# Kernel tuning notes

Hardware: AMD Instinct MI355X
Metric: run time of the kernel (lower is better)

The kernel has to match this reference:

```python
import jax, jax.numpy as jnp
import numpy as np

WS = 7          # window size
DIM = 256       # channels
HEADS = 8       # attention heads
NW = 1024       # windows per image ((224/7)^2)
B = 4           # image batch
N = WS * WS     # tokens per window


def get_relative_position_index(ws):
    # Faithful numpy port of the torch helper for square equal q/k windows.
    coords = np.stack(np.meshgrid(np.arange(ws), np.arange(ws), indexing='ij'))  # (2, ws, ws)
    flat = coords.reshape(2, -1)                                                  # (2, N)
    rel = flat[:, :, None] - flat[:, None, :]                                     # (2, N, N)
    rel = rel.transpose(1, 2, 0).astype(np.int32)                                 # (N, N, 2)
    rel[..., 0] += ws - 1
    rel[..., 1] += ws - 1
    rel[..., 0] *= 2 * ws - 1   # q_windows[1] + k_windows[1] - 1
    return rel.sum(-1)          # (N, N) in [0, (2*ws-1)^2)


def setup_inputs() -> dict:
    key = jax.random.key(0)
    ks = jax.random.split(key, 8)
    B_ = B * NW
    x = jax.random.normal(ks[0], (B_, N, DIM), dtype=jnp.float32)
    mask = jax.random.normal(ks[1], (NW, N, N), dtype=jnp.float32)  # additive window mask
    qkv_w = jax.random.normal(ks[2], (3 * DIM, DIM), dtype=jnp.float32) * (DIM ** -0.5)
    qkv_b = jax.random.normal(ks[3], (3 * DIM,), dtype=jnp.float32) * 0.02
    proj_w = jax.random.normal(ks[4], (DIM, DIM), dtype=jnp.float32) * (DIM ** -0.5)
    proj_b = jax.random.normal(ks[5], (DIM,), dtype=jnp.float32) * 0.02
    rpb_table = jax.random.normal(ks[6], ((2 * WS - 1) ** 2, HEADS), dtype=jnp.float32) * 0.02
    rel_pos_index = jnp.asarray(get_relative_position_index(WS), dtype=jnp.int32)
    return {"x": x, "mask": mask, "qkv_w": qkv_w, "qkv_b": qkv_b,
            "proj_w": proj_w, "proj_b": proj_b,
            "rpb_table": rpb_table, "rel_pos_index": rel_pos_index}


def reference(x, mask, qkv_w, qkv_b, proj_w, proj_b, rpb_table, rel_pos_index):
    B_, n, C = x.shape
    hd = C // HEADS
    scale = hd ** -0.5
    # qkv projection: (B_, N, 3, H, hd) -> (3, B_, H, N, hd)
    qkv = (x @ qkv_w.T + qkv_b).reshape(B_, n, 3, HEADS, hd).transpose(2, 0, 3, 1, 4)
    q, k, v = qkv[0] * scale, qkv[1], qkv[2]
    attn = jnp.einsum('bhnd,bhmd->bhnm', q, k)                  # (B_, H, N, N)
    bias = rpb_table[rel_pos_index].transpose(2, 0, 1)          # gather -> (H, N, N)
    attn = attn + bias[None]
    nW = mask.shape[0]
    attn = attn.reshape(B_ // nW, nW, HEADS, n, n) + mask[None, :, None]
    attn = jax.nn.softmax(attn.reshape(B_, HEADS, n, n), axis=-1)
    out = jnp.einsum('bhnm,bhmd->bhnd', attn, v)                # (B_, H, N, hd)
    out = out.transpose(0, 2, 1, 3).reshape(B_, n, C)
    return out @ proj_w.T + proj_b
```

## Files before the change

kernel.cpp:

```cpp
#include <hip/hip_runtime.h>

typedef short bf16x8 __attribute__((ext_vector_type(8)));
typedef unsigned short u16x8 __attribute__((ext_vector_type(8)));
typedef unsigned short u16x4 __attribute__((ext_vector_type(4)));
typedef float f32x4 __attribute__((ext_vector_type(4)));
typedef unsigned short u16;

#define N_TOK 49
#define DIM   256
#define NWIN  1024
#define XS_S  264
#define QK_S  40
#define VT_S  72
#define P_S   72
#define OH_S  40

#define WS_MASK_OFF   0ull
#define WS_QKVW_OFF   2458624ull
#define WS_PROJW_OFF  (WS_QKVW_OFF + 196608ull)
#define WS_QKVB_OFF   (WS_PROJW_OFF + 65536ull)
#define WS_PROJB_OFF  (WS_QKVB_OFF + 768ull)
#define WS_RPB_OFF    (WS_PROJB_OFF + 256ull)
#define WS_TOT_U16    (WS_RPB_OFF + 1352ull)

__device__ __forceinline__ float bf2f(u16 b) {
  unsigned int u = ((unsigned int)b) << 16;
  return __builtin_bit_cast(float, u);
}
__device__ __forceinline__ u16 f2bf(float f) {
  unsigned int u = __builtin_bit_cast(unsigned int, f);
  return (u16)((u + 0x7fffu + ((u >> 16) & 1u)) >> 16);
}
__device__ __forceinline__ float lde(const void* p, size_t i, bool isbf) {
  return isbf ? bf2f(((const u16*)p)[i]) : ((const float*)p)[i];
}
__device__ __forceinline__ bf16x8 cvt8(const float* f) {
  f32x4 a = *(const f32x4*)f;
  f32x4 b = *(const f32x4*)(f + 4);
  u16x8 r;
  r[0]=f2bf(a[0]); r[1]=f2bf(a[1]); r[2]=f2bf(a[2]); r[3]=f2bf(a[3]);
  r[4]=f2bf(b[0]); r[5]=f2bf(b[1]); r[6]=f2bf(b[2]); r[7]=f2bf(b[3]);
  return __builtin_bit_cast(bf16x8, r);
}
__device__ __forceinline__ bool probe_bf(const void* p) {
  int lane = threadIdx.x & 63;
  u16 h = ((const u16*)p)[2 * lane];
  int e = (h >> 7) & 0xFF;
  bool sane = ((h & 0x7fffu) == 0) || (e >= 96 && e <= 140);
  return (__ballot(!sane) == 0ull);
}

__global__ void cvt_kernel(const void* __restrict__ src, u16* __restrict__ dst, int n) {
  bool isbf = probe_bf(src);
  int i = blockIdx.x * 256 + threadIdx.x;
  if (i < n)
    dst[i] = isbf ? ((const u16*)src)[i] : f2bf(((const float*)src)[i]);
}

__global__ __launch_bounds__(256, 2)
void winattn_kernel(const void* __restrict__ x, const void* __restrict__ mask,
                    const void* __restrict__ qkv_w, const void* __restrict__ qkv_b,
                    const void* __restrict__ proj_w, const void* __restrict__ proj_b,
                    const void* __restrict__ rpb, const int* __restrict__ rel_idx,
                    void* __restrict__ out, const u16* __restrict__ wsu, int use_ws)
{
  __shared__ u16 xs [64 * XS_S];
  __shared__ u16 qs [64 * QK_S];
  __shared__ u16 ksm[64 * QK_S];
  __shared__ u16 vT [32 * VT_S];
  __shared__ u16 Ps [64 * P_S];
  __shared__ u16 oh [64 * OH_S];

  const int tid  = threadIdx.x;
  const int wv   = tid >> 6;
  const int lane = tid & 63;
  const int quad = lane >> 4;
  const int l15  = lane & 15;
  const int w    = blockIdx.x;

  const bool bx = probe_bf(x);
  bool bm0 = probe_bf(mask), bw0 = probe_bf(qkv_w), bqb0 = probe_bf(qkv_b),
       bpw0 = probe_bf(proj_w), bpb0 = probe_bf(proj_b), brp0 = probe_bf(rpb);

  const void* mask_p = use_ws ? (const void*)(wsu + WS_MASK_OFF)  : mask;
  const void* qkvw_p = use_ws ? (const void*)(wsu + WS_QKVW_OFF)  : qkv_w;
  const void* qkvb_p = use_ws ? (const void*)(wsu + WS_QKVB_OFF)  : qkv_b;
  const void* pjw_p  = use_ws ? (const void*)(wsu + WS_PROJW_OFF) : proj_w;
  const void* pjb_p  = use_ws ? (const void*)(wsu + WS_PROJB_OFF) : proj_b;
  const void* rpb_p  = use_ws ? (const void*)(wsu + WS_RPB_OFF)   : rpb;
  const bool bm  = use_ws ? true : bm0;
  const bool bw  = use_ws ? true : bw0;
  const bool bqb = use_ws ? true : bqb0;
  const bool bpw = use_ws ? true : bpw0;
  const bool bpb = use_ws ? true : bpb0;
  const bool brp = use_ws ? true : brp0;

  if (bx) {
    const u16* xw = (const u16*)x + (size_t)w * (N_TOK * DIM);
    for (int c = tid; c < (N_TOK * DIM / 8); c += 256) {
      int t = (c * 8) >> 8, col = (c * 8) & 255;
      *(u16x8*)&xs[t * XS_S + col] = ((const u16x8*)xw)[c];
    }
  } else {
    const float* xw = (const float*)x + (size_t)w * (N_TOK * DIM);
    for (int c = tid; c < (N_TOK * DIM / 8); c += 256) {
      int t = (c * 8) >> 8, col = (c * 8) & 255;
      *(u16x8*)&xs[t * XS_S + col] = __builtin_bit_cast(u16x8, cvt8(xw + c * 8));
    }
  }
  {
    u16x8 z = {0, 0, 0, 0, 0, 0, 0, 0};
    for (int c = tid; c < 495; c += 256)
      *(u16x8*)&xs[N_TOK * XS_S + c * 8] = z;
  }
  __syncthreads();

  f32x4 pacc[16];
  #pragma unroll
  for (int i = 0; i < 16; ++i) pacc[i] = (f32x4){0.f, 0.f, 0.f, 0.f};

  const int    mrow = 16 * wv + quad * 4;
  const size_t moff = (size_t)(w & (NWIN - 1)) * (N_TOK * N_TOK);

  #pragma unroll 1
  for (int h = 0; h < 8; ++h) {
    f32x4 acc[6];
    #pragma unroll
    for (int j = 0; j < 6; ++j) acc[j] = (f32x4){0.f, 0.f, 0.f, 0.f};
    const int  nb0  = h * 32;
    const u16* arow = &xs[(16 * wv + l15) * XS_S + quad * 8];
    if (bw) {
      const u16* wp = (const u16*)qkvw_p;
      #pragma unroll
      for (int ks = 0; ks < 8; ++ks) {
        bf16x8 a = *(const bf16x8*)(arow + ks * 32);
        #pragma unroll
        for (int j = 0; j < 6; ++j) {
          int n = (j >> 1) * 256 + nb0 + (j & 1) * 16 + l15;
          bf16x8 b = *(const bf16x8*)(wp + (size_t)n * DIM + ks * 32 + quad * 8);
          acc[j] = __builtin_amdgcn_mfma_f32_16x16x32_bf16(a, b, acc[j], 0, 0, 0);
        }
      }
    } else {
      const float* wp = (const float*)qkvw_p;
      #pragma unroll
      for (int ks = 0; ks < 8; ++ks) {
        bf16x8 a = *(const bf16x8*)(arow + ks * 32);
        #pragma unroll
        for (int j = 0; j < 6; ++j) {
          int n = (j >> 1) * 256 + nb0 + (j & 1) * 16 + l15;
          bf16x8 b = cvt8(wp + (size_t)n * DIM + ks * 32 + quad * 8);
          acc[j] = __builtin_amdgcn_mfma_f32_16x16x32_bf16(a, b, acc[j], 0, 0, 0);
        }
      }
    }
    {
      const float scale = 0.1767766952966369f;
      #pragma unroll
      for (int j = 0; j < 6; ++j) {
        int   n    = (j >> 1) * 256 + nb0 + (j & 1) * 16 + l15;
        float bias = lde(qkvb_p, n, bqb);
        int   lc   = (j & 1) * 16 + l15;
        if (j < 2) {
          #pragma unroll
          for (int r = 0; r < 4; ++r)
            qs[(mrow + r) * QK_S + lc] = f2bf((acc[j][r] + bias) * scale);
        } else if (j < 4) {
          #pragma unroll
          for (int r = 0; r < 4; ++r)
            ksm[(mrow + r) * QK_S + lc] = f2bf(acc[j][r] + bias);
        } else {
          u16x4 pk;
          #pragma unroll
          for (int r = 0; r < 4; ++r) pk[r] = f2bf(acc[j][r] + bias);
          *(u16x4*)&vT[lc * VT_S + mrow] = pk;
        }
      }
    }
    __syncthreads();

    f32x4 s[4];
    {
      bf16x8 aq = *(const bf16x8*)&qs[(16 * wv + l15) * QK_S + quad * 8];
      #pragma unroll
      for (int ni = 0; ni < 4; ++ni) {
        bf16x8 bk = *(const bf16x8*)&ksm[(ni * 16 + l15) * QK_S + quad * 8];
        s[ni] = __builtin_amdgcn_mfma_f32_16x16x32_bf16(aq, bk, (f32x4){0.f,0.f,0.f,0.f}, 0, 0, 0);
      }
    }
    float rs[4];
    #pragma unroll
    for (int r = 0; r < 4; ++r) {
      int m = mrow + r;
      #pragma unroll
      for (int ni = 0; ni < 4; ++ni) {
        int   n = ni * 16 + l15;
        float v = s[ni][r];
        if (n >= N_TOK) {
          v = -1e30f;
        } else if (m < N_TOK) {
          int idx = rel_idx[m * N_TOK + n];
          v += lde(rpb_p, (size_t)idx * 8 + h, brp) + lde(mask_p, moff + m * N_TOK + n, bm);
        }
        s[ni][r] = v;
      }
      float mx = fmaxf(fmaxf(s[0][r], s[1][r]), fmaxf(s[2][r], s[3][r]));
      #pragma unroll
      for (int d2 = 1; d2 < 16; d2 <<= 1) mx = fmaxf(mx, __shfl_xor(mx, d2));
      float sum = 0.f;
      #pragma unroll
      for (int ni = 0; ni < 4; ++ni) {
        float p = __expf(s[ni][r] - mx);
        s[ni][r] = p;
        sum += p;
      }
      #pragma unroll
      for (int d2 = 1; d2 < 16; d2 <<= 1) sum += __shfl_xor(sum, d2);
      rs[r] = sum;
      #pragma unroll
      for (int ni = 0; ni < 4; ++ni)
        Ps[(mrow + r) * P_S + ni * 16 + l15] = f2bf(s[ni][r]);
    }

    f32x4 o0 = {0.f,0.f,0.f,0.f}, o1 = {0.f,0.f,0.f,0.f};
    #pragma unroll
    for (int ks = 0; ks < 2; ++ks) {
      bf16x8 ap = *(const bf16x8*)&Ps[(16 * wv + l15) * P_S + ks * 32 + quad * 8];
      bf16x8 b0 = *(const bf16x8*)&vT[(l15)      * VT_S + ks * 32 + quad * 8];
      bf16x8 b1 = *(const bf16x8*)&vT[(16 + l15) * VT_S + ks * 32 + quad * 8];
      o0 = __builtin_amdgcn_mfma_f32_16x16x32_bf16(ap, b0, o0, 0, 0, 0);
      o1 = __builtin_amdgcn_mfma_f32_16x16x32_bf16(ap, b1, o1, 0, 0, 0);
    }
    #pragma unroll
    for (int r = 0; r < 4; ++r) {
      float inv = 1.f / rs[r];
      oh[(mrow + r) * OH_S + l15]      = f2bf(o0[r] * inv);
      oh[(mrow + r) * OH_S + 16 + l15] = f2bf(o1[r] * inv);
    }

    {
      bf16x8 ao = *(const bf16x8*)&oh[(16 * wv + l15) * OH_S + quad * 8];
      if (bpw) {
        const u16* pp = (const u16*)pjw_p;
        #pragma unroll
        for (int ni = 0; ni < 16; ++ni) {
          bf16x8 bp = *(const bf16x8*)(pp + (size_t)(ni * 16 + l15) * DIM + h * 32 + quad * 8);
          pacc[ni] = __builtin_amdgcn_mfma_f32_16x16x32_bf16(ao, bp, pacc[ni], 0, 0, 0);
        }
      } else {
        const float* pp = (const float*)pjw_p;
        #pragma unroll
        for (int ni = 0; ni < 16; ++ni) {
          bf16x8 bp = cvt8(pp + (size_t)(ni * 16 + l15) * DIM + h * 32 + quad * 8);
          pacc[ni] = __builtin_amdgcn_mfma_f32_16x16x32_bf16(ao, bp, pacc[ni], 0, 0, 0);
        }
      }
    }
    __syncthreads();
  }

  const size_t obase = (size_t)w * (N_TOK * DIM);
  if (bx) {
    u16* ow = (u16*)out + obase;
    #pragma unroll
    for (int r = 0; r < 4; ++r) {
      int m = mrow + r;
      if (m < N_TOK) {
        #pragma unroll
        for (int ni = 0; ni < 16; ++ni) {
          int col = ni * 16 + l15;
          ow[m * DIM + col] = f2bf(pacc[ni][r] + lde(pjb_p, col, bpb));
        }
      }
    }
  } else {
    float* ow = (float*)out + obase;
    #pragma unroll
    for (int r = 0; r < 4; ++r) {
      int m = mrow + r;
      if (m < N_TOK) {
        #pragma unroll
        for (int ni = 0; ni < 16; ++ni) {
          int col = ni * 16 + l15;
          ow[m * DIM + col] = pacc[ni][r] + lde(pjb_p, col, bpb);
        }
      }
    }
  }
}

extern "C" void kernel_launch(void* const* d_in, const int* in_sizes, int n_in,
                              void* d_out, int out_size, void* d_ws, size_t ws_size,
                              hipStream_t stream) {
  const int use_ws = (ws_size >= WS_TOT_U16 * 2) ? 1 : 0;
  u16* wsu = (u16*)d_ws;
  if (use_ws) {
    auto cv = [&](const void* src, unsigned long long off, int n) {
      cvt_kernel<<<(n + 255) / 256, 256, 0, stream>>>(src, wsu + off, n);
    };
    cv(d_in[1], WS_MASK_OFF,  NWIN * N_TOK * N_TOK);
    cv(d_in[2], WS_QKVW_OFF,  3 * DIM * DIM);
    cv(d_in[3], WS_QKVB_OFF,  3 * DIM);
    cv(d_in[4], WS_PROJW_OFF, DIM * DIM);
    cv(d_in[5], WS_PROJB_OFF, DIM);
    cv(d_in[6], WS_RPB_OFF,   169 * 8);
  }
  winattn_kernel<<<4096, 256, 0, stream>>>(
      d_in[0], d_in[1], d_in[2], d_in[3], d_in[4], d_in[5], d_in[6],
      (const int*)d_in[7], d_out, wsu, use_ws);
}
```

Before: 1.824 ms.

## Precombine mask and position bias per head, keep x in registers, double-buffer QKV

A new preprocessing kernel fuses the window mask and the gathered relative-position bias into one bf16 table per window and head. The attention kernel then loads that table with a single read per element instead of an index gather plus two lookups. The x tile now lives in registers rather than LDS. The q/k/v LDS buffers are double-buffered so the per-head trailing barrier can be removed, and launch bounds rise to 3 blocks per SM. In exchange the bias table is about 39 MB of extra workspace traffic, and register pressure goes up.

```diff
diff --git a/kernel.cpp b/kernel.cpp
--- a/kernel.cpp
+++ b/kernel.cpp
@@ -7,9 +7,9 @@
 typedef unsigned short u16;
 
 #define N_TOK 49
+#define NN    2401
 #define DIM   256
 #define NWIN  1024
-#define XS_S  264
 #define QK_S  40
 #define VT_S  72
 #define P_S   72
@@ -23,6 +23,13 @@
 #define WS_RPB_OFF    (WS_PROJB_OFF + 256ull)
 #define WS_TOT_U16    (WS_RPB_OFF + 1352ull)
 
+#define C2_CMB_OFF    0ull
+#define C2_QKVW_OFF   (1024ull * 8ull * NN)
+#define C2_PROJW_OFF  (C2_QKVW_OFF + 196608ull)
+#define C2_QKVB_OFF   (C2_PROJW_OFF + 65536ull)
+#define C2_PROJB_OFF  (C2_QKVB_OFF + 768ull)
+#define C2_TOT_U16    (C2_PROJB_OFF + 256ull)
+
 __device__ __forceinline__ float bf2f(u16 b) {
   unsigned int u = ((unsigned int)b) << 16;
   return __builtin_bit_cast(float, u);
@@ -57,17 +64,33 @@
     dst[i] = isbf ? ((const u16*)src)[i] : f2bf(((const float*)src)[i]);
 }
 
-__global__ __launch_bounds__(256, 2)
+__global__ void build_bias_kernel(const void* __restrict__ mask, const void* __restrict__ rpb,
+                                  const int* __restrict__ rel_idx, u16* __restrict__ dst) {
+  __shared__ float msk[NN];
+  __shared__ float rp[169 * 8];
+  const int win = blockIdx.x;
+  const bool bm = probe_bf(mask);
+  const bool br = probe_bf(rpb);
+  for (int i = threadIdx.x; i < NN; i += 256) msk[i] = lde(mask, (size_t)win * NN + i, bm);
+  for (int i = threadIdx.x; i < 169 * 8; i += 256) rp[i] = lde(rpb, i, br);
+  __syncthreads();
+  u16* dw = dst + (size_t)win * (8ull * NN);
+  for (int i = threadIdx.x; i < 8 * NN; i += 256) {
+    int h = i / NN, mn = i % NN;
+    dw[i] = f2bf(msk[mn] + rp[rel_idx[mn] * 8 + h]);
+  }
+}
+
+__global__ __launch_bounds__(256, 3)
 void winattn_kernel(const void* __restrict__ x, const void* __restrict__ mask,
                     const void* __restrict__ qkv_w, const void* __restrict__ qkv_b,
                     const void* __restrict__ proj_w, const void* __restrict__ proj_b,
                     const void* __restrict__ rpb, const int* __restrict__ rel_idx,
-                    void* __restrict__ out, const u16* __restrict__ wsu, int use_ws)
+                    void* __restrict__ out, const u16* __restrict__ wsu, int mode)
 {
-  __shared__ u16 xs [64 * XS_S];
-  __shared__ u16 qs [64 * QK_S];
-  __shared__ u16 ksm[64 * QK_S];
-  __shared__ u16 vT [32 * VT_S];
+  __shared__ u16 qs [2][64 * QK_S];
+  __shared__ u16 ksm[2][64 * QK_S];
+  __shared__ u16 vT [2][32 * VT_S];
   __shared__ u16 Ps [64 * P_S];
   __shared__ u16 oh [64 * OH_S];
 
@@ -79,61 +102,95 @@
   const int w    = blockIdx.x;
 
   const bool bx = probe_bf(x);
-  bool bm0 = probe_bf(mask), bw0 = probe_bf(qkv_w), bqb0 = probe_bf(qkv_b),
-       bpw0 = probe_bf(proj_w), bpb0 = probe_bf(proj_b), brp0 = probe_bf(rpb);
-
-  const void* mask_p = use_ws ? (const void*)(wsu + WS_MASK_OFF)  : mask;
-  const void* qkvw_p = use_ws ? (const void*)(wsu + WS_QKVW_OFF)  : qkv_w;
-  const void* qkvb_p = use_ws ? (const void*)(wsu + WS_QKVB_OFF)  : qkv_b;
-  const void* pjw_p  = use_ws ? (const void*)(wsu + WS_PROJW_OFF) : proj_w;
-  const void* pjb_p  = use_ws ? (const void*)(wsu + WS_PROJB_OFF) : proj_b;
-  const void* rpb_p  = use_ws ? (const void*)(wsu + WS_RPB_OFF)   : rpb;
-  const bool bm  = use_ws ? true : bm0;
-  const bool bw  = use_ws ? true : bw0;
-  const bool bqb = use_ws ? true : bqb0;
-  const bool bpw = use_ws ? true : bpw0;
-  const bool bpb = use_ws ? true : bpb0;
-  const bool brp = use_ws ? true : brp0;
-
-  if (bx) {
-    const u16* xw = (const u16*)x + (size_t)w * (N_TOK * DIM);
-    for (int c = tid; c < (N_TOK * DIM / 8); c += 256) {
-      int t = (c * 8) >> 8, col = (c * 8) & 255;
-      *(u16x8*)&xs[t * XS_S + col] = ((const u16x8*)xw)[c];
-    }
-  } else {
-    const float* xw = (const float*)x + (size_t)w * (N_TOK * DIM);
-    for (int c = tid; c < (N_TOK * DIM / 8); c += 256) {
-      int t = (c * 8) >> 8, col = (c * 8) & 255;
-      *(u16x8*)&xs[t * XS_S + col] = __builtin_bit_cast(u16x8, cvt8(xw + c * 8));
-    }
-  }
+  bool bm = true, bw = true, bqb = true, bpw = true, bpb = true, brp = true;
+  if (mode == 0) {
+    bm = probe_bf(mask); bw = probe_bf(qkv_w); bqb = probe_bf(qkv_b);
+    bpw = probe_bf(proj_w); bpb = probe_bf(proj_b); brp = probe_bf(rpb);
+  }
+
+  const void* mask_p = (mode == 1) ? (const void*)(wsu + WS_MASK_OFF) : mask;
+  const void* rpb_p  = (mode == 1) ? (const void*)(wsu + WS_RPB_OFF)  : rpb;
+  const void* qkvw_p = (mode == 2) ? (const void*)(wsu + C2_QKVW_OFF)
+                     : (mode == 1) ? (const void*)(wsu + WS_QKVW_OFF) : qkv_w;
+  const void* qkvb_p = (mode == 2) ? (const void*)(wsu + C2_QKVB_OFF)
+                     : (mode == 1) ? (const void*)(wsu + WS_QKVB_OFF) : qkv_b;
+  const void* pjw_p  = (mode == 2) ? (const void*)(wsu + C2_PROJW_OFF)
+                     : (mode == 1) ? (const void*)(wsu + WS_PROJW_OFF) : proj_w;
+  const void* pjb_p  = (mode == 2) ? (const void*)(wsu + C2_PROJB_OFF)
+                     : (mode == 1) ? (const void*)(wsu + WS_PROJB_OFF) : proj_b;
+
+  bf16x8 xf[8];
   {
-    u16x8 z = {0, 0, 0, 0, 0, 0, 0, 0};
-    for (int c = tid; c < 495; c += 256)
-      *(u16x8*)&xs[N_TOK * XS_S + c * 8] = z;
-  }
-  __syncthreads();
+    const int row = 16 * wv + l15;
+    if (row < N_TOK) {
+      if (bx) {
+        const u16* xw = (const u16*)x + (size_t)w * (N_TOK * DIM) + row * DIM + quad * 8;
+        #pragma unroll
+        for (int ks = 0; ks < 8; ++ks) xf[ks] = *(const bf16x8*)(xw + ks * 32);
+      } else {
+        const float* xw = (const float*)x + (size_t)w * (N_TOK * DIM) + row * DIM + quad * 8;
+        #pragma unroll
+        for (int ks = 0; ks < 8; ++ks) xf[ks] = cvt8(xw + ks * 32);
+      }
+    } else {
+      const bf16x8 z = {0, 0, 0, 0, 0, 0, 0, 0};
+      #pragma unroll
+      for (int ks = 0; ks < 8; ++ks) xf[ks] = z;
+    }
+  }
 
   f32x4 pacc[16];
   #pragma unroll
   for (int i = 0; i < 16; ++i) pacc[i] = (f32x4){0.f, 0.f, 0.f, 0.f};
 
   const int    mrow = 16 * wv + quad * 4;
-  const size_t moff = (size_t)(w & (NWIN - 1)) * (N_TOK * N_TOK);
+  const size_t moff = (size_t)(w & (NWIN - 1)) * NN;
+  const u16*   cmbw = wsu + C2_CMB_OFF + (size_t)(w & (NWIN - 1)) * (8ull * NN);
 
   #pragma unroll 1
   for (int h = 0; h < 8; ++h) {
+    u16* qsb = qs[h & 1];
+    u16* ksb = ksm[h & 1];
+    u16* vtb = vT[h & 1];
+
+    float cb[4][4];
+    if (mode == 2) {
+      const u16* cp = cmbw + (size_t)h * NN;
+      #pragma unroll
+      for (int r = 0; r < 4; ++r) {
+        const int m = mrow + r;
+        #pragma unroll
+        for (int ni = 0; ni < 4; ++ni) {
+          const int n = ni * 16 + l15;
+          cb[r][ni] = (m < N_TOK && n < N_TOK) ? bf2f(cp[m * N_TOK + n]) : 0.f;
+        }
+      }
+    } else {
+      #pragma unroll
+      for (int r = 0; r < 4; ++r) {
+        const int m = mrow + r;
+        #pragma unroll
+        for (int ni = 0; ni < 4; ++ni) {
+          const int n = ni * 16 + l15;
+          float c = 0.f;
+          if (m < N_TOK && n < N_TOK) {
+            int idx = rel_idx[m * N_TOK + n];
+            c = lde(rpb_p, (size_t)idx * 8 + h, brp) + lde(mask_p, moff + m * N_TOK + n, bm);
+          }
+          cb[r][ni] = c;
+        }
+      }
+    }
+
     f32x4 acc[6];
     #pragma unroll
     for (int j = 0; j < 6; ++j) acc[j] = (f32x4){0.f, 0.f, 0.f, 0.f};
-    const int  nb0  = h * 32;
-    const u16* arow = &xs[(16 * wv + l15) * XS_S + quad * 8];
+    const int nb0 = h * 32;
     if (bw) {
       const u16* wp = (const u16*)qkvw_p;
       #pragma unroll
       for (int ks = 0; ks < 8; ++ks) {
-        bf16x8 a = *(const bf16x8*)(arow + ks * 32);
+        bf16x8 a = xf[ks];
         #pragma unroll
         for (int j = 0; j < 6; ++j) {
           int n = (j >> 1) * 256 + nb0 + (j & 1) * 16 + l15;
@@ -145,7 +202,7 @@
       const float* wp = (const float*)qkvw_p;
       #pragma unroll
       for (int ks = 0; ks < 8; ++ks) {
-        bf16x8 a = *(const bf16x8*)(arow + ks * 32);
+        bf16x8 a = xf[ks];
         #pragma unroll
         for (int j = 0; j < 6; ++j) {
           int n = (j >> 1) * 256 + nb0 + (j & 1) * 16 + l15;
@@ -164,16 +221,16 @@
         if (j < 2) {
           #pragma unroll
           for (int r = 0; r < 4; ++r)
-            qs[(mrow + r) * QK_S + lc] = f2bf((acc[j][r] + bias) * scale);
+            qsb[(mrow + r) * QK_S + lc] = f2bf((acc[j][r] + bias) * scale);
         } else if (j < 4) {
           #pragma unroll
           for (int r = 0; r < 4; ++r)
-            ksm[(mrow + r) * QK_S + lc] = f2bf(acc[j][r] + bias);
+            ksb[(mrow + r) * QK_S + lc] = f2bf(acc[j][r] + bias);
         } else {
           u16x4 pk;
           #pragma unroll
           for (int r = 0; r < 4; ++r) pk[r] = f2bf(acc[j][r] + bias);
-          *(u16x4*)&vT[lc * VT_S + mrow] = pk;
+          *(u16x4*)&vtb[lc * VT_S + mrow] = pk;
         }
       }
     }
@@ -181,28 +238,21 @@
 
     f32x4 s[4];
     {
-      bf16x8 aq = *(const bf16x8*)&qs[(16 * wv + l15) * QK_S + quad * 8];
+      bf16x8 aq = *(const bf16x8*)&qsb[(16 * wv + l15) * QK_S + quad * 8];
       #pragma unroll
       for (int ni = 0; ni < 4; ++ni) {
-        bf16x8 bk = *(const bf16x8*)&ksm[(ni * 16 + l15) * QK_S + quad * 8];
+        bf16x8 bk = *(const bf16x8*)&ksb[(ni * 16 + l15) * QK_S + quad * 8];
         s[ni] = __builtin_amdgcn_mfma_f32_16x16x32_bf16(aq, bk, (f32x4){0.f,0.f,0.f,0.f}, 0, 0, 0);
       }
     }
     float rs[4];
     #pragma unroll
     for (int r = 0; r < 4; ++r) {
-      int m = mrow + r;
       #pragma unroll
       for (int ni = 0; ni < 4; ++ni) {
         int   n = ni * 16 + l15;
         float v = s[ni][r];
-        if (n >= N_TOK) {
-          v = -1e30f;
-        } else if (m < N_TOK) {
-          int idx = rel_idx[m * N_TOK + n];
-          v += lde(rpb_p, (size_t)idx * 8 + h, brp) + lde(mask_p, moff + m * N_TOK + n, bm);
-        }
-        s[ni][r] = v;
+        s[ni][r] = (n >= N_TOK) ? -1e30f : v + cb[r][ni];
       }
       float mx = fmaxf(fmaxf(s[0][r], s[1][r]), fmaxf(s[2][r], s[3][r]));
       #pragma unroll
@@ -226,8 +276,8 @@
     #pragma unroll
     for (int ks = 0; ks < 2; ++ks) {
       bf16x8 ap = *(const bf16x8*)&Ps[(16 * wv + l15) * P_S + ks * 32 + quad * 8];
-      bf16x8 b0 = *(const bf16x8*)&vT[(l15)      * VT_S + ks * 32 + quad * 8];
-      bf16x8 b1 = *(const bf16x8*)&vT[(16 + l15) * VT_S + ks * 32 + quad * 8];
+      bf16x8 b0 = *(const bf16x8*)&vtb[(l15)      * VT_S + ks * 32 + quad * 8];
+      bf16x8 b1 = *(const bf16x8*)&vtb[(16 + l15) * VT_S + ks * 32 + quad * 8];
       o0 = __builtin_amdgcn_mfma_f32_16x16x32_bf16(ap, b0, o0, 0, 0, 0);
       o1 = __builtin_amdgcn_mfma_f32_16x16x32_bf16(ap, b1, o1, 0, 0, 0);
     }
@@ -256,7 +306,6 @@
         }
       }
     }
-    __syncthreads();
   }
 
   const size_t obase = (size_t)w * (N_TOK * DIM);
@@ -292,12 +341,23 @@
 extern "C" void kernel_launch(void* const* d_in, const int* in_sizes, int n_in,
                               void* d_out, int out_size, void* d_ws, size_t ws_size,
                               hipStream_t stream) {
-  const int use_ws = (ws_size >= WS_TOT_U16 * 2) ? 1 : 0;
   u16* wsu = (u16*)d_ws;
-  if (use_ws) {
-    auto cv = [&](const void* src, unsigned long long off, int n) {
-      cvt_kernel<<<(n + 255) / 256, 256, 0, stream>>>(src, wsu + off, n);
-    };
+  int mode = 0;
+  if (ws_size >= C2_TOT_U16 * 2) mode = 2;
+  else if (ws_size >= WS_TOT_U16 * 2) mode = 1;
+
+  auto cv = [&](const void* src, unsigned long long off, int n) {
+    cvt_kernel<<<(n + 255) / 256, 256, 0, stream>>>(src, wsu + off, n);
+  };
+
+  if (mode == 2) {
+    build_bias_kernel<<<NWIN, 256, 0, stream>>>(d_in[1], d_in[6], (const int*)d_in[7],
+                                                wsu + C2_CMB_OFF);
+    cv(d_in[2], C2_QKVW_OFF, 3 * DIM * DIM);
+    cv(d_in[3], C2_QKVB_OFF, 3 * DIM);
+    cv(d_in[4], C2_PROJW_OFF, DIM * DIM);
+    cv(d_in[5], C2_PROJB_OFF, DIM);
+  } else if (mode == 1) {
     cv(d_in[1], WS_MASK_OFF,  NWIN * N_TOK * N_TOK);
     cv(d_in[2], WS_QKVW_OFF,  3 * DIM * DIM);
     cv(d_in[3], WS_QKVB_OFF,  3 * DIM);
@@ -307,5 +367,5 @@
   }
   winattn_kernel<<<4096, 256, 0, stream>>>(
       d_in[0], d_in[1], d_in[2], d_in[3], d_in[4], d_in[5], d_in[6],
-      (const int*)d_in[7], d_out, wsu, use_ws);
-}
+      (const int*)d_in[7], d_out, wsu, mode);
+}
```

Result: slower. 2.056 ms (+12.7%).
